# Kernel tuning notes

Measured on AMD Instinct MI355X. Metric: run time of the kernel, lower is better.

Reference implementation:

```python
import jax, jax.numpy as jnp
import numpy as np

N_NODES = 100000

def prelu(x, alpha):
    return jnp.where(x >= 0, x, alpha * x)

def setup_inputs() -> dict:
    key = jax.random.key(0)
    ks = jax.random.split(key, 8)
    N, E, D = N_NODES, 1600000, 128
    AX = jax.random.normal(ks[0], (N, D), dtype=jnp.float32)
    A_row = jax.random.randint(ks[1], (E,), 0, N, dtype=jnp.int32)
    A_col = jax.random.randint(ks[2], (E,), 0, N, dtype=jnp.int32)
    A_val = jax.random.uniform(ks[3], (E,), dtype=jnp.float32)
    # Xavier-uniform linear weights, zero bias (as in module init)
    lim = float(np.sqrt(6.0 / (D + D)))
    Wr_w = jax.random.uniform(ks[4], (D, D), minval=-lim, maxval=lim, dtype=jnp.float32)
    W_w = jax.random.uniform(ks[5], (D, D), minval=-lim, maxval=lim, dtype=jnp.float32)
    Wr_b = jnp.zeros((D,), dtype=jnp.float32)
    W_b = jnp.zeros((D,), dtype=jnp.float32)
    g_alpha = jnp.full((1,), 0.25, dtype=jnp.float32)    # PReLU default init
    act_alpha = jnp.full((1,), 0.25, dtype=jnp.float32)
    return {"AX": AX, "A_row": A_row, "A_col": A_col, "A_val": A_val,
            "Wr_w": Wr_w, "Wr_b": Wr_b, "W_w": W_w, "W_b": W_b,
            "g_alpha": g_alpha, "act_alpha": act_alpha}

def reference(AX, A_row, A_col, A_val, Wr_w, Wr_b, W_w, W_b, g_alpha, act_alpha):
    # h = g(Wr @ AX)  : [N, H]
    h = prelu(AX @ Wr_w.T + Wr_b, g_alpha)
    # SpMM: temp[i] = sum_{(i,j) in E} A_val * h[j]
    msgs = A_val[:, None] * h[A_col]                       # [E, H] gather
    temp = jax.ops.segment_sum(msgs, A_row, num_segments=N_NODES)
    # act(W @ temp), unsqueeze batch dim
    out = prelu(temp @ W_w.T + W_b, act_alpha)
    return out[None, :, :]
```

## Files before the change

kernel.cpp:

```cpp
#include <hip/hip_runtime.h>
#include <stdint.h>


typedef _Float16 half8 __attribute__((ext_vector_type(8)));
typedef _Float16 half4 __attribute__((ext_vector_type(4)));
typedef _Float16 half2v __attribute__((ext_vector_type(2)));
typedef float floatx4 __attribute__((ext_vector_type(4)));

#define LDK 136
#define SHIFT 5
#define NBMAX 3200
#define NBLK 256
#define SCT 1024
#define CAP 1024

__global__ __launch_bounds__(256, 2)
void gemm128_prelu(const float* __restrict__ X, const float* __restrict__ W,
                   const float* __restrict__ bias, const float* __restrict__ alpha_p,
                   _Float16* __restrict__ out, int N)
{
    __shared__ _Float16 Xs[128 * LDK];
    __shared__ _Float16 Ws[128 * LDK];
    const int tid = threadIdx.x;
    const int bm  = blockIdx.x * 128;
    const float alpha = *alpha_p;

#pragma unroll
    for (int i = 0; i < 16; ++i) {
        int c   = tid + i * 256;
        int row = c >> 5;
        int coff = (c & 31) * 4;
        float4 f = *(const float4*)(W + row * 128 + coff);
        half4 hv = { (_Float16)f.x, (_Float16)f.y, (_Float16)f.z, (_Float16)f.w };
        *(half4*)(&Ws[row * LDK + coff]) = hv;
    }
#pragma unroll
    for (int i = 0; i < 16; ++i) {
        int c   = tid + i * 256;
        int row = c >> 5;
        int coff = (c & 31) * 4;
        int grow = bm + row;
        half4 hv = {};
        if (grow < N) {
            float4 f = *(const float4*)(X + (size_t)grow * 128 + coff);
            hv[0] = (_Float16)f.x; hv[1] = (_Float16)f.y;
            hv[2] = (_Float16)f.z; hv[3] = (_Float16)f.w;
        }
        *(half4*)(&Xs[row * LDK + coff]) = hv;
    }
    __syncthreads();

    const int wave = tid >> 6;
    const int lane = tid & 63;
    const int l15  = lane & 15;
    const int quad = lane >> 4;

    floatx4 acc[2][8] = {};
#pragma unroll
    for (int k0 = 0; k0 < 128; k0 += 32) {
        half8 a0 = *(const half8*)(&Xs[(wave * 32 +      l15) * LDK + k0 + quad * 8]);
        half8 a1 = *(const half8*)(&Xs[(wave * 32 + 16 + l15) * LDK + k0 + quad * 8]);
        half8 b[8];
#pragma unroll
        for (int n = 0; n < 8; ++n)
            b[n] = *(const half8*)(&Ws[(n * 16 + l15) * LDK + k0 + quad * 8]);
#pragma unroll
        for (int n = 0; n < 8; ++n) {
            acc[0][n] = __builtin_amdgcn_mfma_f32_16x16x32_f16(a0, b[n], acc[0][n], 0, 0, 0);
            acc[1][n] = __builtin_amdgcn_mfma_f32_16x16x32_f16(a1, b[n], acc[1][n], 0, 0, 0);
        }
    }

#pragma unroll
    for (int mt = 0; mt < 2; ++mt) {
#pragma unroll
        for (int n = 0; n < 8; ++n) {
#pragma unroll
            for (int r = 0; r < 4; ++r) {
                int row = bm + wave * 32 + mt * 16 + quad * 4 + r;
                int col = n * 16 + l15;
                if (row < N) {
                    float v = acc[mt][n][r] + bias[col];
                    v = (v >= 0.f) ? v : alpha * v;
                    out[(size_t)row * 128 + col] = (_Float16)v;
                }
            }
        }
    }
}

__global__ __launch_bounds__(SCT)
void bucket_hist(const int* __restrict__ rows, int* __restrict__ hist_g,
                 int E, int chunk, int NB,
                 const float* __restrict__ W, _Float16* __restrict__ W16)
{
    __shared__ int lh[NBMAX];
    int tid = threadIdx.x, blk = blockIdx.x;
    if (blk == 0) {
#pragma unroll
        for (int j = 0; j < 16; ++j) W16[tid + j * 1024] = (_Float16)W[tid + j * 1024];
    }
    for (int i = tid; i < NB; i += SCT) lh[i] = 0;
    __syncthreads();
    int s = blk * chunk, e = min(E, s + chunk);
    for (int i = s + tid; i < e; i += SCT)
        atomicAdd(&lh[rows[i] >> SHIFT], 1);
    __syncthreads();
    for (int b = tid; b < NB; b += SCT)
        hist_g[b * NBLK + blk] = lh[b];
}

__global__ __launch_bounds__(NBLK)
void bucket_scan1(int* __restrict__ hist_g, int* __restrict__ tot)
{
    __shared__ int sd[NBLK];
    int b = blockIdx.x, t = threadIdx.x;
    int v = hist_g[b * NBLK + t];
    sd[t] = v;
    __syncthreads();
    for (int off = 1; off < NBLK; off <<= 1) {
        int x = (t >= off) ? sd[t - off] : 0;
        __syncthreads();
        sd[t] += x;
        __syncthreads();
    }
    hist_g[b * NBLK + t] = sd[t] - v;
    if (t == NBLK - 1) tot[b] = sd[t];
}

__global__ __launch_bounds__(1024)
void bucket_scan2(const int* __restrict__ tot, int* __restrict__ bkt_ptr, int NB, int E)
{
    __shared__ int sd[1024];
    int t = threadIdx.x;
    int v[4]; int s = 0;
#pragma unroll
    for (int j = 0; j < 4; ++j) {
        int idx = t * 4 + j;
        v[j] = (idx < NB) ? tot[idx] : 0;
        s += v[j];
    }
    sd[t] = s;
    __syncthreads();
    for (int off = 1; off < 1024; off <<= 1) {
        int x = (t >= off) ? sd[t - off] : 0;
        __syncthreads();
        sd[t] += x;
        __syncthreads();
    }
    int base = (t == 0) ? 0 : sd[t - 1];
#pragma unroll
    for (int j = 0; j < 4; ++j) {
        int idx = t * 4 + j;
        if (idx < NB) { bkt_ptr[idx] = base; base += v[j]; }
    }
    if (t == 0) bkt_ptr[NB] = E;
}

__global__ __launch_bounds__(SCT)
void bucket_scatter(const int* __restrict__ rows, const int* __restrict__ cols,
                    const float* __restrict__ vals, const int* __restrict__ bkt_ptr,
                    const int* __restrict__ hist_g, uint2* __restrict__ edges,
                    int E, int chunk, int NB)
{
    __shared__ int cur[NBMAX];
    int tid = threadIdx.x, blk = blockIdx.x;
    for (int b = tid; b < NB; b += SCT)
        cur[b] = bkt_ptr[b] + hist_g[b * NBLK + blk];
    __syncthreads();
    int s = blk * chunk, e = min(E, s + chunk);
    for (int i = s + tid; i < e; i += SCT) {
        int r = rows[i];
        int b = r >> SHIFT;
        uint2 ed;
        ed.x = (unsigned)cols[i] | ((unsigned)(r & 31) << 20);
        ed.y = __float_as_uint(vals[i]);
        int p = atomicAdd(&cur[b], 1);
        edges[p] = ed;
    }
}

__global__ __launch_bounds__(256, 8)
void spmm_fused(const int* __restrict__ bkt_ptr, const uint2* __restrict__ edges,
                const _Float16* __restrict__ h, const _Float16* __restrict__ W16,
                const float* __restrict__ bias, const float* __restrict__ alpha_p,
                float* __restrict__ out, int N)
{
    __shared__ uint2 eS[CAP];
    __shared__ _Float16 T[32 * LDK];
    __shared__ int bins[32], startS[33];

    const int tid  = threadIdx.x;
    const int wave = tid >> 6;
    const int lane = tid & 63;
    const int b    = blockIdx.x;
    const int s0   = bkt_ptr[b], e0 = bkt_ptr[b + 1];

    float acc[8][2] = {};

    for (int base = s0; base < e0; base += CAP) {
        const int n = min(CAP, e0 - base);
        if (tid < 32) bins[tid] = 0;
        __syncthreads();
        uint2 q[4];
#pragma unroll
        for (int u = 0; u < 4; ++u) {
            int i = tid + u * 256;
            if (i < n) {
                q[u] = edges[base + i];
                atomicAdd(&bins[q[u].x >> 20], 1);
            }
        }
        __syncthreads();
        if (tid < 32) {
            int x = bins[tid];
#pragma unroll
            for (int off = 1; off < 32; off <<= 1) {
                int y = __shfl_up(x, off);
                if (tid >= off) x += y;
            }
            startS[tid + 1] = x;
            if (tid == 0) startS[0] = 0;
            bins[tid] = x - bins[tid];
        }
        __syncthreads();
#pragma unroll
        for (int u = 0; u < 4; ++u) {
            int i = tid + u * 256;
            if (i < n) {
                int p = atomicAdd(&bins[q[u].x >> 20], 1);
                eS[p] = q[u];
            }
        }
        __syncthreads();

#pragma unroll
        for (int j = 0; j < 8; ++j) {
            int r  = wave * 8 + j;
            int rs = startS[r], re = startS[r + 1];
            float a0r = acc[j][0], a1r = acc[j][1];
            int i = rs;
            for (; i + 7 < re; i += 8) {
                uint2 q0 = eS[i],     q1 = eS[i + 1], q2 = eS[i + 2], q3 = eS[i + 3];
                uint2 q4 = eS[i + 4], q5 = eS[i + 5], q6 = eS[i + 6], q7 = eS[i + 7];
                half2v v0 = *(const half2v*)(h + (size_t)(q0.x & 0xFFFFF) * 128 + lane * 2);
                half2v v1 = *(const half2v*)(h + (size_t)(q1.x & 0xFFFFF) * 128 + lane * 2);
                half2v v2 = *(const half2v*)(h + (size_t)(q2.x & 0xFFFFF) * 128 + lane * 2);
                half2v v3 = *(const half2v*)(h + (size_t)(q3.x & 0xFFFFF) * 128 + lane * 2);
                half2v v4 = *(const half2v*)(h + (size_t)(q4.x & 0xFFFFF) * 128 + lane * 2);
                half2v v5 = *(const half2v*)(h + (size_t)(q5.x & 0xFFFFF) * 128 + lane * 2);
                half2v v6 = *(const half2v*)(h + (size_t)(q6.x & 0xFFFFF) * 128 + lane * 2);
                half2v v7 = *(const half2v*)(h + (size_t)(q7.x & 0xFFFFF) * 128 + lane * 2);
                float w0 = __uint_as_float(q0.y), w1 = __uint_as_float(q1.y);
                float w2 = __uint_as_float(q2.y), w3 = __uint_as_float(q3.y);
                float w4 = __uint_as_float(q4.y), w5 = __uint_as_float(q5.y);
                float w6 = __uint_as_float(q6.y), w7 = __uint_as_float(q7.y);
                a0r += w0 * (float)v0[0]; a1r += w0 * (float)v0[1];
                a0r += w1 * (float)v1[0]; a1r += w1 * (float)v1[1];
                a0r += w2 * (float)v2[0]; a1r += w2 * (float)v2[1];
                a0r += w3 * (float)v3[0]; a1r += w3 * (float)v3[1];
                a0r += w4 * (float)v4[0]; a1r += w4 * (float)v4[1];
                a0r += w5 * (float)v5[0]; a1r += w5 * (float)v5[1];
                a0r += w6 * (float)v6[0]; a1r += w6 * (float)v6[1];
                a0r += w7 * (float)v7[0]; a1r += w7 * (float)v7[1];
            }
            for (; i + 1 < re; i += 2) {
                uint2 q0 = eS[i], q1 = eS[i + 1];
                half2v v0 = *(const half2v*)(h + (size_t)(q0.x & 0xFFFFF) * 128 + lane * 2);
                half2v v1 = *(const half2v*)(h + (size_t)(q1.x & 0xFFFFF) * 128 + lane * 2);
                float w0 = __uint_as_float(q0.y), w1 = __uint_as_float(q1.y);
                a0r += w0 * (float)v0[0]; a1r += w0 * (float)v0[1];
                a0r += w1 * (float)v1[0]; a1r += w1 * (float)v1[1];
            }
            if (i < re) {
                uint2 q0 = eS[i];
                half2v v0 = *(const half2v*)(h + (size_t)(q0.x & 0xFFFFF) * 128 + lane * 2);
                float w0 = __uint_as_float(q0.y);
                a0r += w0 * (float)v0[0]; a1r += w0 * (float)v0[1];
            }
            acc[j][0] = a0r; acc[j][1] = a1r;
        }
        __syncthreads();
    }

#pragma unroll
    for (int j = 0; j < 8; ++j) {
        half2v o = { (_Float16)acc[j][0], (_Float16)acc[j][1] };
        *(half2v*)(&T[(wave * 8 + j) * LDK + lane * 2]) = o;
    }
    __syncthreads();

    const float alpha = *alpha_p;
    const int l15  = lane & 15;
    const int quad = lane >> 4;
    floatx4 c[2][2] = {};
#pragma unroll
    for (int k0 = 0; k0 < 128; k0 += 32) {
        half8 a0 = *(const half8*)(&T[(     l15) * LDK + k0 + quad * 8]);
        half8 a1 = *(const half8*)(&T[(16 + l15) * LDK + k0 + quad * 8]);
#pragma unroll
        for (int nt = 0; nt < 2; ++nt) {
            int nrow = (wave * 2 + nt) * 16 + l15;
            half8 bf = *(const half8*)(W16 + nrow * 128 + k0 + quad * 8);
            c[0][nt] = __builtin_amdgcn_mfma_f32_16x16x32_f16(a0, bf, c[0][nt], 0, 0, 0);
            c[1][nt] = __builtin_amdgcn_mfma_f32_16x16x32_f16(a1, bf, c[1][nt], 0, 0, 0);
        }
    }
    const int row0 = b << SHIFT;
#pragma unroll
    for (int mt = 0; mt < 2; ++mt) {
#pragma unroll
        for (int nt = 0; nt < 2; ++nt) {
            int col = (wave * 2 + nt) * 16 + l15;
            float bcol = bias[col];
#pragma unroll
            for (int r = 0; r < 4; ++r) {
                int row = row0 + mt * 16 + quad * 4 + r;
                if (row < N) {
                    float v = c[mt][nt][r] + bcol;
                    v = (v >= 0.f) ? v : alpha * v;
                    out[(size_t)row * 128 + col] = v;
                }
            }
        }
    }
}

static inline size_t align256(size_t x) { return (x + 255) & ~(size_t)255; }

extern "C" void kernel_launch(void* const* d_in, const int* in_sizes, int n_in,
                              void* d_out, int out_size, void* d_ws, size_t ws_size,
                              hipStream_t stream)
{
    const float* AX        = (const float*)d_in[0];
    const int*   A_row     = (const int*)  d_in[1];
    const int*   A_col     = (const int*)  d_in[2];
    const float* A_val     = (const float*)d_in[3];
    const float* Wr_w      = (const float*)d_in[4];
    const float* Wr_b      = (const float*)d_in[5];
    const float* W_w       = (const float*)d_in[6];
    const float* W_b       = (const float*)d_in[7];
    const float* g_alpha   = (const float*)d_in[8];
    const float* act_alpha = (const float*)d_in[9];

    const int N = in_sizes[0] / 128;
    const int E = in_sizes[1];
    const int NB = (N + 31) >> SHIFT;
    const int chunk = (E + NBLK - 1) / NBLK;

    char* ws = (char*)d_ws;
    size_t off = 0;
    _Float16* h      = (_Float16*)(ws + off); off += align256((size_t)N * 128 * 2);
    uint2*    edges  = (uint2*)   (ws + off); off += align256((size_t)E * 8);
    int*      hist_g = (int*)     (ws + off); off += align256((size_t)NB * NBLK * 4);
    int*      tot    = (int*)     (ws + off); off += align256((size_t)NB * 4);
    int*      bkt_ptr= (int*)     (ws + off); off += align256((size_t)(NB + 1) * 4);
    _Float16* W16    = (_Float16*)(ws + off); off += align256((size_t)128 * 128 * 2);
    (void)ws_size; (void)n_in; (void)out_size;

    const int gemm_grid = (N + 127) / 128;

    gemm128_prelu<<<gemm_grid, 256, 0, stream>>>(AX, Wr_w, Wr_b, g_alpha, h, N);

    bucket_hist<<<NBLK, SCT, 0, stream>>>(A_row, hist_g, E, chunk, NB, W_w, W16);
    bucket_scan1<<<NB, NBLK, 0, stream>>>(hist_g, tot);
    bucket_scan2<<<1, 1024, 0, stream>>>(tot, bkt_ptr, NB, E);
    bucket_scatter<<<NBLK, SCT, 0, stream>>>(A_row, A_col, A_val, bkt_ptr, hist_g, edges, E, chunk, NB);

    spmm_fused<<<NB, 256, 0, stream>>>(bkt_ptr, edges, h, W16, W_b, act_alpha,
                                       (float*)d_out, N);
}
```

Measured before the change: 286.6 us.

## Fuse histogram into GEMM launch and merge two scan kernels via last-block counter

The bucket histogram now runs as extra blocks in the same launch as the first GEMM, so the two independent phases share one grid and can overlap. The two scan kernels are merged: the last block to finish, found with an atomic done-counter, does the final scan of the bucket totals. Together this removes two launches and the gaps between them. In exchange the histogram runs with 256 threads per block, the hist_g layout is transposed, and the final scan runs serially in one 256-thread block with 13 elements per thread.

New measurement: 679.8 us. 137% more time.

```diff
diff --git a/kernel.cpp b/kernel.cpp
--- a/kernel.cpp
+++ b/kernel.cpp
@@ -15,13 +15,37 @@
 #define CAP 1024
 
 __global__ __launch_bounds__(256, 2)
-void gemm128_prelu(const float* __restrict__ X, const float* __restrict__ W,
-                   const float* __restrict__ bias, const float* __restrict__ alpha_p,
-                   _Float16* __restrict__ out, int N)
+void gemm_hist(const float* __restrict__ X, const float* __restrict__ Wr,
+               const float* __restrict__ bias, const float* __restrict__ alpha_p,
+               _Float16* __restrict__ out, int N, int gemmB,
+               const int* __restrict__ rows, int* __restrict__ hist_g,
+               int E, int chunk, int NB,
+               const float* __restrict__ W, _Float16* __restrict__ W16,
+               unsigned* __restrict__ done_ctr)
 {
     __shared__ _Float16 Xs[128 * LDK];
     __shared__ _Float16 Ws[128 * LDK];
     const int tid = threadIdx.x;
+
+    if (blockIdx.x >= gemmB) {
+        const int hb = blockIdx.x - gemmB;
+        int* lh = (int*)Xs;
+        if (hb == 0) {
+            if (tid == 0) *done_ctr = 0;
+            for (int j = 0; j < 64; ++j)
+                W16[tid + j * 256] = (_Float16)W[tid + j * 256];
+        }
+        for (int i = tid; i < NB; i += 256) lh[i] = 0;
+        __syncthreads();
+        int s = hb * chunk, e = min(E, s + chunk);
+        for (int i = s + tid; i < e; i += 256)
+            atomicAdd(&lh[rows[i] >> SHIFT], 1);
+        __syncthreads();
+        for (int b = tid; b < NB; b += 256)
+            hist_g[hb * NB + b] = lh[b];
+        return;
+    }
+
     const int bm  = blockIdx.x * 128;
     const float alpha = *alpha_p;
 
@@ -30,7 +54,7 @@
         int c   = tid + i * 256;
         int row = c >> 5;
         int coff = (c & 31) * 4;
-        float4 f = *(const float4*)(W + row * 128 + coff);
+        float4 f = *(const float4*)(Wr + row * 128 + coff);
         half4 hv = { (_Float16)f.x, (_Float16)f.y, (_Float16)f.z, (_Float16)f.w };
         *(half4*)(&Ws[row * LDK + coff]) = hv;
     }
@@ -89,33 +113,16 @@
     }
 }
 
-__global__ __launch_bounds__(SCT)
-void bucket_hist(const int* __restrict__ rows, int* __restrict__ hist_g,
-                 int E, int chunk, int NB,
-                 const float* __restrict__ W, _Float16* __restrict__ W16)
-{
-    __shared__ int lh[NBMAX];
-    int tid = threadIdx.x, blk = blockIdx.x;
-    if (blk == 0) {
-#pragma unroll
-        for (int j = 0; j < 16; ++j) W16[tid + j * 1024] = (_Float16)W[tid + j * 1024];
-    }
-    for (int i = tid; i < NB; i += SCT) lh[i] = 0;
-    __syncthreads();
-    int s = blk * chunk, e = min(E, s + chunk);
-    for (int i = s + tid; i < e; i += SCT)
-        atomicAdd(&lh[rows[i] >> SHIFT], 1);
-    __syncthreads();
-    for (int b = tid; b < NB; b += SCT)
-        hist_g[b * NBLK + blk] = lh[b];
-}
-
 __global__ __launch_bounds__(NBLK)
-void bucket_scan1(int* __restrict__ hist_g, int* __restrict__ tot)
+void scan_fused(int* __restrict__ hist_g, int* __restrict__ tot,
+                int* __restrict__ bkt_ptr, int NB, int E,
+                unsigned* __restrict__ done_ctr)
 {
     __shared__ int sd[NBLK];
-    int b = blockIdx.x, t = threadIdx.x;
-    int v = hist_g[b * NBLK + t];
+    __shared__ unsigned isLast;
+    const int b = blockIdx.x, t = threadIdx.x;
+
+    int v = hist_g[t * NB + b];
     sd[t] = v;
     __syncthreads();
     for (int off = 1; off < NBLK; off <<= 1) {
@@ -124,25 +131,25 @@
         sd[t] += x;
         __syncthreads();
     }
-    hist_g[b * NBLK + t] = sd[t] - v;
+    hist_g[t * NB + b] = sd[t] - v;
     if (t == NBLK - 1) tot[b] = sd[t];
-}
-
-__global__ __launch_bounds__(1024)
-void bucket_scan2(const int* __restrict__ tot, int* __restrict__ bkt_ptr, int NB, int E)
-{
-    __shared__ int sd[1024];
-    int t = threadIdx.x;
-    int v[4]; int s = 0;
-#pragma unroll
-    for (int j = 0; j < 4; ++j) {
-        int idx = t * 4 + j;
-        v[j] = (idx < NB) ? tot[idx] : 0;
-        s += v[j];
+
+    __threadfence();
+    if (t == 0) isLast = (atomicAdd(done_ctr, 1u) == (unsigned)(gridDim.x - 1));
+    __syncthreads();
+    if (!isLast) return;
+    __threadfence();
+
+    int v2[13]; int s = 0;
+#pragma unroll
+    for (int j = 0; j < 13; ++j) {
+        int idx = t * 13 + j;
+        v2[j] = (idx < NB) ? tot[idx] : 0;
+        s += v2[j];
     }
     sd[t] = s;
     __syncthreads();
-    for (int off = 1; off < 1024; off <<= 1) {
+    for (int off = 1; off < NBLK; off <<= 1) {
         int x = (t >= off) ? sd[t - off] : 0;
         __syncthreads();
         sd[t] += x;
@@ -150,9 +157,9 @@
     }
     int base = (t == 0) ? 0 : sd[t - 1];
 #pragma unroll
-    for (int j = 0; j < 4; ++j) {
-        int idx = t * 4 + j;
-        if (idx < NB) { bkt_ptr[idx] = base; base += v[j]; }
+    for (int j = 0; j < 13; ++j) {
+        int idx = t * 13 + j;
+        if (idx < NB) { bkt_ptr[idx] = base; base += v2[j]; }
     }
     if (t == 0) bkt_ptr[NB] = E;
 }
@@ -166,7 +173,7 @@
     __shared__ int cur[NBMAX];
     int tid = threadIdx.x, blk = blockIdx.x;
     for (int b = tid; b < NB; b += SCT)
-        cur[b] = bkt_ptr[b] + hist_g[b * NBLK + blk];
+        cur[b] = bkt_ptr[b] + hist_g[blk * NB + b];
     __syncthreads();
     int s = blk * chunk, e = min(E, s + chunk);
     for (int i = s + tid; i < e; i += SCT) {
@@ -350,23 +357,23 @@
 
     char* ws = (char*)d_ws;
     size_t off = 0;
-    _Float16* h      = (_Float16*)(ws + off); off += align256((size_t)N * 128 * 2);
-    uint2*    edges  = (uint2*)   (ws + off); off += align256((size_t)E * 8);
-    int*      hist_g = (int*)     (ws + off); off += align256((size_t)NB * NBLK * 4);
-    int*      tot    = (int*)     (ws + off); off += align256((size_t)NB * 4);
-    int*      bkt_ptr= (int*)     (ws + off); off += align256((size_t)(NB + 1) * 4);
-    _Float16* W16    = (_Float16*)(ws + off); off += align256((size_t)128 * 128 * 2);
+    _Float16* h       = (_Float16*)(ws + off); off += align256((size_t)N * 128 * 2);
+    uint2*    edges   = (uint2*)   (ws + off); off += align256((size_t)E * 8);
+    int*      hist_g  = (int*)     (ws + off); off += align256((size_t)NB * NBLK * 4);
+    int*      tot     = (int*)     (ws + off); off += align256((size_t)NB * 4);
+    int*      bkt_ptr = (int*)     (ws + off); off += align256((size_t)(NB + 1) * 4);
+    _Float16* W16     = (_Float16*)(ws + off); off += align256((size_t)128 * 128 * 2);
+    unsigned* done_ctr= (unsigned*)(ws + off); off += align256(4);
     (void)ws_size; (void)n_in; (void)out_size;
 
-    const int gemm_grid = (N + 127) / 128;
-
-    gemm128_prelu<<<gemm_grid, 256, 0, stream>>>(AX, Wr_w, Wr_b, g_alpha, h, N);
-
-    bucket_hist<<<NBLK, SCT, 0, stream>>>(A_row, hist_g, E, chunk, NB, W_w, W16);
-    bucket_scan1<<<NB, NBLK, 0, stream>>>(hist_g, tot);
-    bucket_scan2<<<1, 1024, 0, stream>>>(tot, bkt_ptr, NB, E);
-    bucket_scatter<<<NBLK, SCT, 0, stream>>>(A_row, A_col, A_val, bkt_ptr, hist_g, edges, E, chunk, NB);
-
+    const int gemmB = (N + 127) / 128;
+
+    gemm_hist<<<gemmB + NBLK, 256, 0, stream>>>(AX, Wr_w, Wr_b, g_alpha, h, N, gemmB,
+                                                A_row, hist_g, E, chunk, NB,
+                                                W_w, W16, done_ctr);
+    scan_fused<<<NB, NBLK, 0, stream>>>(hist_g, tot, bkt_ptr, NB, E, done_ctr);
+    bucket_scatter<<<NBLK, SCT, 0, stream>>>(A_row, A_col, A_val, bkt_ptr, hist_g,
+                                             edges, E, chunk, NB);
     spmm_fused<<<NB, 256, 0, stream>>>(bkt_ptr, edges, h, W16, W_b, act_alpha,
                                        (float*)d_out, N);
 }
```
